# Kernel optimization log

Hardware: AMD Instinct MI355X
Metric: run time of the kernel (lower is better)

The kernel has to match this reference:

```python
import jax, jax.numpy as jnp
import numpy as np

VARIANCES = jnp.array([0.1, 0.1, 0.2, 0.2], jnp.float32)
TOTAL_LABELS = 81
MAX_TOTAL = 200        # max_total_size (also max_output_size_per_class)
SCORE_T = 0.5          # score_threshold
IOU_T = 0.5            # tf combined_non_max_suppression default iou_threshold


def setup_inputs() -> dict:
    key = jax.random.key(0)
    k1, k2, k3, k4 = jax.random.split(key, 4)
    B, N, C = 8, 1000, TOTAL_LABELS
    # valid normalized RoIs: y1,x1 in [0,0.7), h,w in [0.01,0.31)
    yx1 = jax.random.uniform(k1, (B, N, 2), jnp.float32) * 0.7
    hw = jax.random.uniform(k2, (B, N, 2), jnp.float32) * 0.3 + 0.01
    roi_bboxes = jnp.concatenate([yx1, yx1 + hw], axis=-1)  # [y1,x1,y2,x2]
    pred_deltas = jax.random.normal(k3, (B, N, C * 4), jnp.float32) * 0.5
    pred_label_probs = jax.random.uniform(k4, (B, N, C), jnp.float32)
    return {"roi_bboxes": roi_bboxes, "pred_deltas": pred_deltas,
            "pred_label_probs": pred_label_probs}


def _decode(rois, deltas):
    # rois: [..., 4] (y1,x1,y2,x2); deltas: [..., 4] (dy,dx,dh,dw)
    h = rois[..., 2] - rois[..., 0]
    w = rois[..., 3] - rois[..., 1]
    cy = rois[..., 0] + 0.5 * h
    cx = rois[..., 1] + 0.5 * w
    ncy = deltas[..., 0] * h + cy
    ncx = deltas[..., 1] * w + cx
    nh = jnp.exp(deltas[..., 2]) * h
    nw = jnp.exp(deltas[..., 3]) * w
    return jnp.stack([ncy - 0.5 * nh, ncx - 0.5 * nw,
                      ncy + 0.5 * nh, ncx + 0.5 * nw], axis=-1)


def _nms_lane(boxes, scores):
    # greedy per-class NMS over one (batch, class) lane. boxes [N,4], scores [N]
    N = boxes.shape[0]
    order = jnp.argsort(-scores)
    b = boxes[order]
    s = scores[order]
    area = (b[:, 2] - b[:, 0]) * (b[:, 3] - b[:, 1])
    idx = jnp.arange(N)

    def body(i, keep):
        bi = b[i]
        iy1 = jnp.maximum(bi[0], b[:, 0])
        ix1 = jnp.maximum(bi[1], b[:, 1])
        iy2 = jnp.minimum(bi[2], b[:, 2])
        ix2 = jnp.minimum(bi[3], b[:, 3])
        inter = jnp.maximum(iy2 - iy1, 0.0) * jnp.maximum(ix2 - ix1, 0.0)
        iou = inter / (area[i] + area - inter + 1e-8)
        suppress = keep[i] & (iou > IOU_T) & (idx > i)
        return keep & ~suppress

    keep0 = s > SCORE_T                       # score filtering before NMS
    keep = jax.lax.fori_loop(0, N, body, keep0)
    keep = keep & (jnp.cumsum(keep) <= MAX_TOTAL)  # max_output_size_per_class
    return b, jnp.where(keep, s, 0.0)          # boxes in score order, masked scores


def _forward(roi_bboxes, pred_deltas, pred_label_probs):
    B, N, _ = pred_deltas.shape
    C = TOTAL_LABELS
    deltas = pred_deltas.reshape(B, N, C, 4) * VARIANCES
    boxes = _decode(roi_bboxes[:, :, None, :], deltas)          # [B,N,C,4]
    bg = jnp.argmax(pred_label_probs, axis=-1)[..., None] == 0  # background rows
    scores = jnp.where(bg, 0.0, pred_label_probs)               # [B,N,C]

    boxes_t = boxes.transpose(0, 2, 1, 3)   # [B,C,N,4]
    scores_t = scores.transpose(0, 2, 1)    # [B,C,N]
    b_s, s_s = jax.vmap(jax.vmap(_nms_lane))(boxes_t, scores_t)

    flat_s = s_s.reshape(B, C * N)
    flat_b = b_s.reshape(B, C * N, 4)
    cls = jnp.broadcast_to(jnp.arange(C)[:, None], (C, N)).reshape(C * N)

    top_s, top_i = jax.lax.top_k(flat_s, MAX_TOTAL)             # combined top-k
    top_b = jnp.take_along_axis(flat_b, top_i[..., None], axis=1)
    top_c = cls[top_i]

    valid = top_s > 0.0
    final_b = jnp.clip(jnp.where(valid[..., None], top_b, 0.0), 0.0, 1.0)
    final_c = jnp.where(valid, top_c, 0).astype(jnp.float32)
    final_s = jnp.where(valid, top_s, 0.0)
    return final_b, final_c, final_s


def reference(roi_bboxes, pred_deltas, pred_label_probs):
    return _forward(roi_bboxes, pred_deltas, pred_label_probs)
```

## Files before the change

kernel.cpp:

```cpp
#include <hip/hip_runtime.h>

#define NROI 1000
#define NCLS 81
#define NB   8
#define NLANE (NB*NCLS)
#define MAXM 1024
#define MAXKEEP 200
#define SCORE_T 0.5f
#define NT 512
#define NW 8
#define HBITS 13
#define HSIZE (1<<HBITS)
#define SCAP 1024

typedef unsigned long long u64;
typedef unsigned int u32;


__device__ __forceinline__ void decode_box(const float* __restrict__ roi,
                                           const float* __restrict__ dl,
                                           float& oy1, float& ox1,
                                           float& oy2, float& ox2) {
#pragma clang fp contract(off)
  float y1 = roi[0], x1 = roi[1], y2 = roi[2], x2 = roi[3];
  float h = y2 - y1;
  float w = x2 - x1;
  float cy = y1 + 0.5f * h;
  float cx = x1 + 0.5f * w;
  float d0 = dl[0] * 0.1f;
  float d1 = dl[1] * 0.1f;
  float d2 = dl[2] * 0.2f;
  float d3 = dl[3] * 0.2f;
  float ncy = d0 * h + cy;
  float ncx = d1 * w + cx;
  float nh = expf(d2) * h;
  float nw = expf(d3) * w;
  oy1 = ncy - 0.5f * nh;
  ox1 = ncx - 0.5f * nw;
  oy2 = ncy + 0.5f * nh;
  ox2 = ncx + 0.5f * nw;
}

__device__ __forceinline__ float area_f(float4 bx) {
#pragma clang fp contract(off)
  return (bx.z - bx.x) * (bx.w - bx.y);
}

__device__ __forceinline__ bool hit_f(float4 bi, float ia, float4 bj, float ja) {
#pragma clang fp contract(off)
  float yy1 = fmaxf(bi.x, bj.x);
  float xx1 = fmaxf(bi.y, bj.y);
  float yy2 = fminf(bi.z, bj.z);
  float xx2 = fminf(bi.w, bj.w);
  float ih = fmaxf(yy2 - yy1, 0.0f);
  float iw = fmaxf(xx2 - xx1, 0.0f);
  float inter = ih * iw;
  float den = ia + ja;
  den = den - inter;
  den = den + 1e-8f;
  return (inter + inter) > den;
}

__device__ __forceinline__ u64 pack_key(u32 sbits, int flat, int n) {
  return ((u64)sbits << 32) | ((u64)(131071 - flat) << 15) | ((u64)n << 5);
}

__global__ __launch_bounds__(256) void bg_kernel(const float* __restrict__ probs,
                                                 int* __restrict__ bg,
                                                 int* __restrict__ bhist) {
  if (blockIdx.x < 64) {
    int base = blockIdx.x * 1024 + threadIdx.x;
#pragma unroll
    for (int r = 0; r < 4; ++r) bhist[base + (r << 8)] = 0;
  }
  int row = blockIdx.x * 4 + (threadIdx.x >> 6);
  int lane = threadIdx.x & 63;
  if (row >= NB * NROI) return;
  const float* p = probs + (size_t)row * NCLS;
  float m = -1e30f;
  for (int idx = 1 + lane; idx < NCLS; idx += 64) m = fmaxf(m, p[idx]);
  for (int off = 32; off; off >>= 1) m = fmaxf(m, __shfl_xor(m, off));
  if (lane == 0) bg[row] = (p[0] >= m) ? 1 : 0;
}

__global__ __launch_bounds__(NT) void gather_nms_kernel(
    const float* __restrict__ roi, const float* __restrict__ deltas,
    const float* __restrict__ probs, const int* __restrict__ bg,
    int* __restrict__ keep_count, u64* __restrict__ lane_key,
    int* __restrict__ bhist) {
  int lane = (blockIdx.x % 8) * NCLS + blockIdx.x / 8;
  int b = lane / NCLS, c = lane % NCLS;
  int tid = threadIdx.x;
  int w = tid >> 6, l = tid & 63;

  __shared__ alignas(16) char smem[26624];
  float4* sbox   = (float4*)smem;
  u64*    skeyU  = (u64*)smem;
  u64*    skeyB  = (u64*)(smem + 8192);
  u64*    skey   = (u64*)(smem + 16384);
  int*    bcnt   = (int*)(smem + 24576);
  int*    bstart = (int*)(smem + 25600);
  __shared__ u64 hmask8[NW][64];
  __shared__ u64 suppm8[NW];
  __shared__ u64 keepmask[16];
  __shared__ int scount, segbase[16];

  if (tid == 0) scount = 0;
  if (tid < 256) bcnt[tid] = 0;
  __syncthreads();

  for (int base_n = 0; base_n < NROI; base_n += NT) {
    int n = base_n + tid;
    bool cand = false;
    float s = 0.0f;
    if (n < NROI) {
      int row = b * NROI + n;
      s = probs[(size_t)row * NCLS + c];
      cand = (s > SCORE_T) && (bg[row] == 0);
    }
    u64 bal = __ballot(cand);
    int wb = 0;
    if (l == 0) wb = atomicAdd(&scount, (int)__popcll(bal));
    wb = __shfl(wb, 0);
    if (cand) {
      int off = (int)__popcll(bal & ((1ull << l) - 1ull));
      u32 sb = __float_as_uint(s);
      skeyU[wb + off] = ((u64)sb << 32) | (u64)(0xFFFFFFFFu - (u32)n);
      atomicAdd(&bcnt[(sb >> 15) & 255], 1);
    }
  }
  __syncthreads();
  int M = scount;
  int nchunks = (M + 63) >> 6;

  if (w == 0) {
    int d0 = 4 * l, d1 = d0 + 1, d2 = d0 + 2, d3 = d0 + 3;
    int c0 = bcnt[255 - d0], c1 = bcnt[255 - d1];
    int c2 = bcnt[255 - d2], c3 = bcnt[255 - d3];
    int t = c0 + c1 + c2 + c3;
    int inc = t;
    for (int off = 1; off < 64; off <<= 1) {
      int v = __shfl_up(inc, off);
      if (l >= off) inc += v;
    }
    int excl = inc - t;
    int s0 = excl, s1 = excl + c0, s2 = excl + c0 + c1, s3 = excl + c0 + c1 + c2;
    bcnt[255 - d0] = s0; bstart[255 - d0] = s0;
    bcnt[255 - d1] = s1; bstart[255 - d1] = s1;
    bcnt[255 - d2] = s2; bstart[255 - d2] = s2;
    bcnt[255 - d3] = s3; bstart[255 - d3] = s3;
  }
  __syncthreads();

  for (int p = tid; p < M; p += NT) {
    u64 k = skeyU[p];
    int bkt = (int)((k >> 47) & 255);
    int pos = atomicAdd(&bcnt[bkt], 1);
    skeyB[pos] = k;
  }
  __syncthreads();

  for (int p = tid; p < M; p += NT) {
    u64 k = skeyB[p];
    int bkt = (int)((k >> 47) & 255);
    int st = bstart[bkt], en = bcnt[bkt];
    int r = st;
    for (int q = st; q < en; ++q) r += (skeyB[q] > k) ? 1 : 0;
    skey[r] = k;
  }
  if (tid < 16) {
    int rem = M - (tid << 6);
    keepmask[tid] = (rem >= 64) ? ~0ull : ((rem <= 0) ? 0ull : ((1ull << rem) - 1ull));
  }
  __syncthreads();

  if (w == 7 && nchunks > 0) {
    u64 k = skey[l];
    int nn = (int)(0xFFFFFFFFu - (u32)(k & 0xFFFFFFFFull));
    int row = b * NROI + ((l < M) ? nn : 0);
    float by1, bx1, by2, bx2;
    decode_box(roi + (size_t)row * 4, deltas + ((size_t)row * NCLS + c) * 4,
               by1, bx1, by2, bx2);
    sbox[l] = make_float4(by1, bx1, by2, bx2);
  }
  __syncthreads();

  int kc = 0;
  const u64 stridemask = 0x0101010101010101ull << w;
  const u64 low = (1ull << l) - 1ull;
  for (int ck = 0; ck < nchunks; ++ck) {
    int start = ck << 6;
    float4 bj = sbox[start + l];
    float ja = area_f(bj);

    {
      u64 part = 0;
#pragma unroll
      for (int r = 0; r < 8; ++r) {
        int i = (w << 3) + r;
        float4 bi = sbox[start + i];
        float ia = area_f(bi);
        if (hit_f(bi, ia, bj, ja)) part |= (1ull << i);
      }
      hmask8[w][l] = part;
    }

    {
      bool supp = false;
      for (int q = 0; q < ck; ++q) {
        u64 mq = keepmask[q] & stridemask;
        while (mq) {
          int i = __ffsll((unsigned long long)mq) - 1;
          mq &= mq - 1;
          float4 bi = sbox[(q << 6) + i];
          float ia = area_f(bi);
          supp |= hit_f(bi, ia, bj, ja);
        }
      }
      u64 sb = __ballot(supp);
      if (l == 0) suppm8[w] = sb;
    }

    if (w == 7 && ck + 1 < nchunks) {
      int p = ((ck + 1) << 6) + l;
      u64 k = skey[p];
      int nn = (int)(0xFFFFFFFFu - (u32)(k & 0xFFFFFFFFull));
      int row = b * NROI + ((p < M) ? nn : 0);
      float by1, bx1, by2, bx2;
      decode_box(roi + (size_t)row * 4, deltas + ((size_t)row * NCLS + c) * 4,
                 by1, bx1, by2, bx2);
      sbox[p] = make_float4(by1, bx1, by2, bx2);
    }
    __syncthreads();

    u64 rowm = hmask8[0][l] | hmask8[1][l] | hmask8[2][l] | hmask8[3][l]
             | hmask8[4][l] | hmask8[5][l] | hmask8[6][l] | hmask8[7][l];
    u64 sall = suppm8[0] | suppm8[1] | suppm8[2] | suppm8[3]
             | suppm8[4] | suppm8[5] | suppm8[6] | suppm8[7];
    int rem0 = M - start;
    u64 alive = (rem0 >= 64) ? ~0ull : ((rem0 <= 0) ? 0ull : ((1ull << rem0) - 1ull));
    u64 und = alive & ~sall;
    u64 kept = 0;
    while (und) {
      bool isu = (und >> l) & 1;
      bool su = isu && ((rowm & kept & low) != 0ull);
      bool ke = isu && ((rowm & (kept | und) & low) == 0ull);
      u64 sm = __ballot(su);
      u64 km2 = __ballot(ke);
      kept |= km2;
      und &= ~(sm | km2);
    }
    if (tid == 0) keepmask[ck] = kept;
    kc += (int)__popcll(kept);
    if (kc >= MAXKEEP) break;
    __syncthreads();
  }
  __syncthreads();

  if (tid < 16) {
    int acc = 0;
    for (int i = 0; i < tid; ++i) acc += (int)__popcll(keepmask[i]);
    segbase[tid] = acc;
  }
  __syncthreads();
  int total = segbase[15] + (int)__popcll(keepmask[15]);
  for (int s = 0; s < 2; ++s) {
    int seg = (w << 1) + s;
    u64 word = keepmask[seg];
    int p = (seg << 6) + l;
    if ((word >> l) & 1) {
      int rank = segbase[seg] + (int)__popcll(word & ((1ull << l) - 1ull));
      if (rank < MAXKEEP) {
        u64 k = skey[p];
        u32 sbits = (u32)(k >> 32);
        int n = (int)(0xFFFFFFFFu - (u32)(k & 0xFFFFFFFFull));
        lane_key[(size_t)lane * MAXKEEP + rank] = pack_key(sbits, c * NROI + p, n);
        atomicAdd(&bhist[b * HSIZE + (int)((sbits >> 10) & (HSIZE - 1))], 1);
      }
    }
  }
  if (tid == 0) keep_count[lane] = min(total, MAXKEEP);
}

__global__ __launch_bounds__(512) void merge_kernel(
    const float* __restrict__ roi, const float* __restrict__ deltas,
    const int* __restrict__ keep_count, const u64* __restrict__ lane_key,
    const int* __restrict__ bhist,
    float* __restrict__ out_b, float* __restrict__ out_c, float* __restrict__ out_s) {
  int b = blockIdx.x;
  int tid = threadIdx.x;
  int w = tid >> 6, l = tid & 63;

  __shared__ int hist[HSIZE];
  __shared__ int hsuf[HSIZE];
  __shared__ int hcur[HSIZE];
  __shared__ int csum[256];
  __shared__ int cnts[NCLS];
  __shared__ int total_sh, scnt_sh;
  __shared__ u64 surv[SCAP];

  for (int i = tid; i < HSIZE; i += 512) hist[i] = bhist[b * HSIZE + i];
  for (int i = tid; i < NCLS; i += 512) cnts[i] = keep_count[b * NCLS + i];
  if (tid == 0) scnt_sh = 0;
  for (int t = tid; t < MAXKEEP; t += 512) {
    size_t ob = ((size_t)b * MAXKEEP + t) * 4;
    out_b[ob + 0] = 0.0f; out_b[ob + 1] = 0.0f;
    out_b[ob + 2] = 0.0f; out_b[ob + 3] = 0.0f;
    out_c[b * MAXKEEP + t] = 0.0f;
    out_s[b * MAXKEEP + t] = 0.0f;
  }
  __syncthreads();

  if (tid < 256) {
    int base = tid * 32;
    int psum = 0;
    for (int i = 0; i < 32; ++i) psum += hist[base + i];
    csum[tid] = psum;
  }
  __syncthreads();
  if (w == 0) {
    int g0 = 4 * l;
    int c0 = csum[g0], c1 = csum[g0 + 1], c2 = csum[g0 + 2], c3 = csum[g0 + 3];
    int t = c0 + c1 + c2 + c3;
    int acc = t;
    for (int off = 1; off < 64; off <<= 1) {
      int v = __shfl_down(acc, off);
      if (l + off < 64) acc += v;
    }
    if (l == 0) total_sh = acc;
    int above = acc - t;
    csum[g0 + 3] = above;
    csum[g0 + 2] = above + c3;
    csum[g0 + 1] = above + c3 + c2;
    csum[g0 + 0] = above + c3 + c2 + c1;
  }
  __syncthreads();
  if (tid < 256) {
    int base = tid * 32;
    int acc = csum[tid];
    for (int i = 31; i >= 0; --i) {
      hsuf[base + i] = acc;
      hcur[base + i] = acc;
      acc += hist[base + i];
    }
  }
  __syncthreads();
  int total = total_sh;
  int valid = (total < MAXKEEP) ? total : MAXKEEP;

  for (int s = tid; s < NCLS * MAXKEEP; s += 512) {
    int c = s / MAXKEEP, h = s % MAXKEEP;
    if (h < cnts[c]) {
      u64 k = lane_key[((size_t)(b * NCLS + c)) * MAXKEEP + h];
      int bkt = (int)((k >> 42) & (HSIZE - 1));
      if (hsuf[bkt] < MAXKEEP) {
        int pos = atomicAdd(&hcur[bkt], 1);
        if (pos < SCAP) { surv[pos] = k; atomicAdd(&scnt_sh, 1); }
      }
    }
  }
  __syncthreads();
  int scnt = min(scnt_sh, SCAP);

  for (int p = tid; p < scnt; p += 512) {
    u64 k = surv[p];
    int bkt = (int)((k >> 42) & (HSIZE - 1));
    int st = hsuf[bkt];
    int en = st + hist[bkt];
    if (en > SCAP) en = SCAP;
    int r = st;
    for (int q = st; q < en; ++q) r += (surv[q] > k) ? 1 : 0;
    if (r < valid) {
      int flat = 131071 - (int)((k >> 15) & 0x1FFFF);
      int c = flat / NROI;
      int n = (int)((k >> 5) & 0x3FF);
      int row = b * NROI + n;
      float by1, bx1, by2, bx2;
      decode_box(roi + (size_t)row * 4, deltas + ((size_t)row * NCLS + c) * 4,
                 by1, bx1, by2, bx2);
      size_t ob = ((size_t)b * MAXKEEP + r) * 4;
      out_b[ob + 0] = fminf(fmaxf(by1, 0.0f), 1.0f);
      out_b[ob + 1] = fminf(fmaxf(bx1, 0.0f), 1.0f);
      out_b[ob + 2] = fminf(fmaxf(by2, 0.0f), 1.0f);
      out_b[ob + 3] = fminf(fmaxf(bx2, 0.0f), 1.0f);
      out_c[b * MAXKEEP + r] = (float)c;
      out_s[b * MAXKEEP + r] = __uint_as_float((u32)(k >> 32));
    }
  }
}

extern "C" void kernel_launch(void* const* d_in, const int* in_sizes, int n_in,
                              void* d_out, int out_size, void* d_ws, size_t ws_size,
                              hipStream_t stream) {
  const float* roi    = (const float*)d_in[0];
  const float* deltas = (const float*)d_in[1];
  const float* probs  = (const float*)d_in[2];

  char* ws = (char*)d_ws;
  int* bg         = (int*)(ws);
  int* keep_count = (int*)(ws + 32768);
  int* bhist      = (int*)(ws + 40960);
  u64* lane_key   = (u64*)(ws + 40960 + 262144);

  float* out_b = (float*)d_out;
  float* out_c = out_b + NB * MAXKEEP * 4;
  float* out_s = out_c + NB * MAXKEEP;

  bg_kernel<<<(NB * NROI + 3) / 4, 256, 0, stream>>>(probs, bg, bhist);
  gather_nms_kernel<<<NLANE, NT, 0, stream>>>(roi, deltas, probs, bg,
                                              keep_count, lane_key, bhist);
  merge_kernel<<<NB, 512, 0, stream>>>(roi, deltas, keep_count, lane_key, bhist,
                                       out_b, out_c, out_s);
}
```

Before: 66.12 us.

## Transpose probs in prep kernel and fuse merge into last NMS block per batch

Replaces the background kernel with a prep kernel that tiles probs rows, computes the background flag, and writes a class-major transposed and masked score array, so each NMS lane reads scores contiguously. The separate merge kernel is removed: the last NMS block to finish for each batch, found through an atomic done counter and threadfence, runs the top-k merge. The histogram shrinks from 8192 to 256 buckets to fit in reused shared memory. This saves one launch and the strided score reads, but adds an extra global write and read of the transposed probs and coarser buckets in the merge rank pass.

Measured after the change: 141.4 us. 114% more time.

```diff
diff --git a/kernel.cpp b/kernel.cpp
--- a/kernel.cpp
+++ b/kernel.cpp
@@ -9,9 +9,8 @@
 #define SCORE_T 0.5f
 #define NT 512
 #define NW 8
-#define HBITS 13
-#define HSIZE (1<<HBITS)
 #define SCAP 1024
+#define TROWS 125
 
 typedef unsigned long long u64;
 typedef unsigned int u32;
@@ -65,29 +64,45 @@
   return ((u64)sbits << 32) | ((u64)(131071 - flat) << 15) | ((u64)n << 5);
 }
 
-__global__ __launch_bounds__(256) void bg_kernel(const float* __restrict__ probs,
-                                                 int* __restrict__ bg,
-                                                 int* __restrict__ bhist) {
-  if (blockIdx.x < 64) {
-    int base = blockIdx.x * 1024 + threadIdx.x;
-#pragma unroll
-    for (int r = 0; r < 4; ++r) bhist[base + (r << 8)] = 0;
-  }
-  int row = blockIdx.x * 4 + (threadIdx.x >> 6);
-  int lane = threadIdx.x & 63;
-  if (row >= NB * NROI) return;
-  const float* p = probs + (size_t)row * NCLS;
-  float m = -1e30f;
-  for (int idx = 1 + lane; idx < NCLS; idx += 64) m = fmaxf(m, p[idx]);
-  for (int off = 32; off; off >>= 1) m = fmaxf(m, __shfl_xor(m, off));
-  if (lane == 0) bg[row] = (p[0] >= m) ? 1 : 0;
+__global__ __launch_bounds__(512) void prep_kernel(const float* __restrict__ probs,
+                                                   float* __restrict__ probs_t,
+                                                   int* __restrict__ bhist,
+                                                   int* __restrict__ done) {
+  __shared__ float tile[TROWS * NCLS];
+  __shared__ u32 bgf[TROWS];
+  int blk = blockIdx.x;
+  int tid = threadIdx.x;
+  if (blk == 0) {
+    for (int i = tid; i < NB * 256; i += 512) bhist[i] = 0;
+    if (tid < NB) done[tid] = 0;
+  }
+  int row0 = blk * TROWS;
+  for (int i = tid; i < TROWS * NCLS; i += 512)
+    tile[i] = probs[(size_t)row0 * NCLS + i];
+  __syncthreads();
+  if (tid < TROWS) {
+    const float* r = &tile[tid * NCLS];
+    float p0 = r[0], m = -1e30f;
+    for (int c2 = 1; c2 < NCLS; ++c2) m = fmaxf(m, r[c2]);
+    bgf[tid] = (p0 >= m) ? 1u : 0u;
+  }
+  __syncthreads();
+  int b = row0 / NROI;
+  int nbase = row0 - b * NROI;
+  for (int j = tid; j < TROWS * NCLS; j += 512) {
+    int c2 = j / TROWS, r = j - c2 * TROWS;
+    float v = bgf[r] ? 0.0f : tile[r * NCLS + c2];
+    probs_t[((size_t)(b * NCLS + c2)) * NROI + nbase + r] = v;
+  }
 }
 
 __global__ __launch_bounds__(NT) void gather_nms_kernel(
     const float* __restrict__ roi, const float* __restrict__ deltas,
-    const float* __restrict__ probs, const int* __restrict__ bg,
+    const float* __restrict__ probs_t,
     int* __restrict__ keep_count, u64* __restrict__ lane_key,
-    int* __restrict__ bhist) {
+    int* __restrict__ bhist, int* __restrict__ done,
+    float* __restrict__ out_b, float* __restrict__ out_c,
+    float* __restrict__ out_s) {
   int lane = (blockIdx.x % 8) * NCLS + blockIdx.x / 8;
   int b = lane / NCLS, c = lane % NCLS;
   int tid = threadIdx.x;
@@ -103,21 +118,17 @@
   __shared__ u64 hmask8[NW][64];
   __shared__ u64 suppm8[NW];
   __shared__ u64 keepmask[16];
-  __shared__ int scount, segbase[16];
+  __shared__ int scount, segbase[16], lastf;
 
   if (tid == 0) scount = 0;
   if (tid < 256) bcnt[tid] = 0;
   __syncthreads();
 
+  const float* pc = probs_t + ((size_t)(b * NCLS + c)) * NROI;
   for (int base_n = 0; base_n < NROI; base_n += NT) {
     int n = base_n + tid;
-    bool cand = false;
-    float s = 0.0f;
-    if (n < NROI) {
-      int row = b * NROI + n;
-      s = probs[(size_t)row * NCLS + c];
-      cand = (s > SCORE_T) && (bg[row] == 0);
-    }
+    float s = (n < NROI) ? pc[n] : 0.0f;
+    bool cand = s > SCORE_T;
     u64 bal = __ballot(cand);
     int wb = 0;
     if (l == 0) wb = atomicAdd(&scount, (int)__popcll(bal));
@@ -275,34 +286,31 @@
         u32 sbits = (u32)(k >> 32);
         int n = (int)(0xFFFFFFFFu - (u32)(k & 0xFFFFFFFFull));
         lane_key[(size_t)lane * MAXKEEP + rank] = pack_key(sbits, c * NROI + p, n);
-        atomicAdd(&bhist[b * HSIZE + (int)((sbits >> 10) & (HSIZE - 1))], 1);
+        atomicAdd(&bhist[b * 256 + (int)((sbits >> 15) & 255)], 1);
       }
     }
   }
   if (tid == 0) keep_count[lane] = min(total, MAXKEEP);
-}
-
-__global__ __launch_bounds__(512) void merge_kernel(
-    const float* __restrict__ roi, const float* __restrict__ deltas,
-    const int* __restrict__ keep_count, const u64* __restrict__ lane_key,
-    const int* __restrict__ bhist,
-    float* __restrict__ out_b, float* __restrict__ out_c, float* __restrict__ out_s) {
-  int b = blockIdx.x;
-  int tid = threadIdx.x;
-  int w = tid >> 6, l = tid & 63;
-
-  __shared__ int hist[HSIZE];
-  __shared__ int hsuf[HSIZE];
-  __shared__ int hcur[HSIZE];
-  __shared__ int csum[256];
-  __shared__ int cnts[NCLS];
-  __shared__ int total_sh, scnt_sh;
-  __shared__ u64 surv[SCAP];
-
-  for (int i = tid; i < HSIZE; i += 512) hist[i] = bhist[b * HSIZE + i];
-  for (int i = tid; i < NCLS; i += 512) cnts[i] = keep_count[b * NCLS + i];
-  if (tid == 0) scnt_sh = 0;
-  for (int t = tid; t < MAXKEEP; t += 512) {
+  __syncthreads();
+  __threadfence();
+  __syncthreads();
+  if (tid == 0) lastf = atomicAdd(&done[b], 1);
+  __syncthreads();
+  if (lastf != NCLS - 1) return;
+  __threadfence();
+
+  int* mhist = (int*)smem;
+  int* mhsuf = (int*)(smem + 1024);
+  int* mhcur = (int*)(smem + 2048);
+  int* mcnts = (int*)(smem + 3072);
+  u64* msurv = (u64*)(smem + 4096);
+  __shared__ int mtot, mscnt;
+  __syncthreads();
+
+  if (tid < 256) mhist[tid] = bhist[b * 256 + tid];
+  for (int i = tid; i < NCLS; i += NT) mcnts[i] = keep_count[b * NCLS + i];
+  if (tid == 0) mscnt = 0;
+  for (int t = tid; t < MAXKEEP; t += NT) {
     size_t ob = ((size_t)b * MAXKEEP + t) * 4;
     out_b[ob + 0] = 0.0f; out_b[ob + 1] = 0.0f;
     out_b[ob + 2] = 0.0f; out_b[ob + 3] = 0.0f;
@@ -311,79 +319,62 @@
   }
   __syncthreads();
 
-  if (tid < 256) {
-    int base = tid * 32;
-    int psum = 0;
-    for (int i = 0; i < 32; ++i) psum += hist[base + i];
-    csum[tid] = psum;
-  }
-  __syncthreads();
   if (w == 0) {
     int g0 = 4 * l;
-    int c0 = csum[g0], c1 = csum[g0 + 1], c2 = csum[g0 + 2], c3 = csum[g0 + 3];
+    int c0 = mhist[g0], c1 = mhist[g0 + 1], c2 = mhist[g0 + 2], c3 = mhist[g0 + 3];
     int t = c0 + c1 + c2 + c3;
     int acc = t;
     for (int off = 1; off < 64; off <<= 1) {
       int v = __shfl_down(acc, off);
       if (l + off < 64) acc += v;
     }
-    if (l == 0) total_sh = acc;
+    if (l == 0) mtot = acc;
     int above = acc - t;
-    csum[g0 + 3] = above;
-    csum[g0 + 2] = above + c3;
-    csum[g0 + 1] = above + c3 + c2;
-    csum[g0 + 0] = above + c3 + c2 + c1;
-  }
-  __syncthreads();
-  if (tid < 256) {
-    int base = tid * 32;
-    int acc = csum[tid];
-    for (int i = 31; i >= 0; --i) {
-      hsuf[base + i] = acc;
-      hcur[base + i] = acc;
-      acc += hist[base + i];
-    }
-  }
-  __syncthreads();
-  int total = total_sh;
-  int valid = (total < MAXKEEP) ? total : MAXKEEP;
-
-  for (int s = tid; s < NCLS * MAXKEEP; s += 512) {
-    int c = s / MAXKEEP, h = s % MAXKEEP;
-    if (h < cnts[c]) {
-      u64 k = lane_key[((size_t)(b * NCLS + c)) * MAXKEEP + h];
-      int bkt = (int)((k >> 42) & (HSIZE - 1));
-      if (hsuf[bkt] < MAXKEEP) {
-        int pos = atomicAdd(&hcur[bkt], 1);
-        if (pos < SCAP) { surv[pos] = k; atomicAdd(&scnt_sh, 1); }
+    int s3 = above, s2 = above + c3, s1 = above + c3 + c2, s0 = above + c3 + c2 + c1;
+    mhsuf[g0 + 3] = s3; mhcur[g0 + 3] = s3;
+    mhsuf[g0 + 2] = s2; mhcur[g0 + 2] = s2;
+    mhsuf[g0 + 1] = s1; mhcur[g0 + 1] = s1;
+    mhsuf[g0 + 0] = s0; mhcur[g0 + 0] = s0;
+  }
+  __syncthreads();
+  int valid = (mtot < MAXKEEP) ? mtot : MAXKEEP;
+
+  for (int s = tid; s < NCLS * MAXKEEP; s += NT) {
+    int c2 = s / MAXKEEP, h = s % MAXKEEP;
+    if (h < mcnts[c2]) {
+      u64 k = lane_key[((size_t)(b * NCLS + c2)) * MAXKEEP + h];
+      int bkt = (int)((k >> 47) & 255);
+      if (mhsuf[bkt] < MAXKEEP) {
+        int pos = atomicAdd(&mhcur[bkt], 1);
+        if (pos < SCAP) { msurv[pos] = k; atomicAdd(&mscnt, 1); }
       }
     }
   }
   __syncthreads();
-  int scnt = min(scnt_sh, SCAP);
-
-  for (int p = tid; p < scnt; p += 512) {
-    u64 k = surv[p];
-    int bkt = (int)((k >> 42) & (HSIZE - 1));
-    int st = hsuf[bkt];
-    int en = st + hist[bkt];
+  int scnt = min(mscnt, SCAP);
+
+  for (int p = tid; p < scnt; p += NT) {
+    u64 k = msurv[p];
+    int bkt = (int)((k >> 47) & 255);
+    int st = mhsuf[bkt];
+    int en = st + mhist[bkt];
     if (en > SCAP) en = SCAP;
     int r = st;
-    for (int q = st; q < en; ++q) r += (surv[q] > k) ? 1 : 0;
+    for (int q = st; q < en; ++q) r += (msurv[q] > k) ? 1 : 0;
     if (r < valid) {
       int flat = 131071 - (int)((k >> 15) & 0x1FFFF);
-      int c = flat / NROI;
+      int c2 = flat / NROI;
       int n = (int)((k >> 5) & 0x3FF);
       int row = b * NROI + n;
       float by1, bx1, by2, bx2;
-      decode_box(roi + (size_t)row * 4, deltas + ((size_t)row * NCLS + c) * 4,
+      decode_box(roi + (size_t)row * 4, deltas + ((size_t)row * NCLS + c2) * 4,
                  by1, bx1, by2, bx2);
       size_t ob = ((size_t)b * MAXKEEP + r) * 4;
       out_b[ob + 0] = fminf(fmaxf(by1, 0.0f), 1.0f);
       out_b[ob + 1] = fminf(fmaxf(bx1, 0.0f), 1.0f);
       out_b[ob + 2] = fminf(fmaxf(by2, 0.0f), 1.0f);
       out_b[ob + 3] = fminf(fmaxf(bx2, 0.0f), 1.0f);
-      out_c[b * MAXKEEP + r] = (float)c;
+      out_c[b * MAXKEEP + r] = (float)c2;
       out_s[b * MAXKEEP + r] = __uint_as_float((u32)(k >> 32));
     }
   }
@@ -397,18 +388,18 @@
   const float* probs  = (const float*)d_in[2];
 
   char* ws = (char*)d_ws;
-  int* bg         = (int*)(ws);
-  int* keep_count = (int*)(ws + 32768);
-  int* bhist      = (int*)(ws + 40960);
-  u64* lane_key   = (u64*)(ws + 40960 + 262144);
+  int*   done       = (int*)(ws);
+  int*   bhist      = (int*)(ws + 4096);
+  int*   keep_count = (int*)(ws + 16384);
+  u64*   lane_key   = (u64*)(ws + 20480);
+  float* probs_t    = (float*)(ws + 1060864);
 
   float* out_b = (float*)d_out;
   float* out_c = out_b + NB * MAXKEEP * 4;
   float* out_s = out_c + NB * MAXKEEP;
 
-  bg_kernel<<<(NB * NROI + 3) / 4, 256, 0, stream>>>(probs, bg, bhist);
-  gather_nms_kernel<<<NLANE, NT, 0, stream>>>(roi, deltas, probs, bg,
-                                              keep_count, lane_key, bhist);
-  merge_kernel<<<NB, 512, 0, stream>>>(roi, deltas, keep_count, lane_key, bhist,
-                                       out_b, out_c, out_s);
-}
+  prep_kernel<<<64, 512, 0, stream>>>(probs, probs_t, bhist, done);
+  gather_nms_kernel<<<NLANE, NT, 0, stream>>>(roi, deltas, probs_t,
+                                              keep_count, lane_key, bhist, done,
+                                              out_b, out_c, out_s);
+}
```
